# Optimization experiments

Measured on AMD Instinct MI355X. Metric: run time of the kernel, lower is better.

## Reference

```python
import jax, jax.numpy as jnp
import numpy as np

H = 4          # attention heads
C = 64         # per-head channels (hidden_size)
NEG_SLOPE = 0.2  # PyG GATConv default negative_slope


def _gat_layer(x, W, a_src, a_dst, b, src, dst):
    """PyG-style GATConv (concat=True) on one graph. x: [N, F]."""
    N = x.shape[0]
    h = (x @ W).reshape(N, H, C)                      # [N, H, C]
    s_src = jnp.sum(h * a_src, axis=-1)               # [N, H]
    s_dst = jnp.sum(h * a_dst, axis=-1)               # [N, H]
    e = jax.nn.leaky_relu(s_src[src] + s_dst[dst], NEG_SLOPE)   # [E, H]
    # softmax over incoming edges of each destination node
    m = jax.ops.segment_max(e, dst, num_segments=N)   # [N, H]
    m = jnp.where(jnp.isfinite(m), m, 0.0)
    ex = jnp.exp(e - m[dst])
    denom = jax.ops.segment_sum(ex, dst, num_segments=N)
    alpha = ex / denom[dst]                           # [E, H]
    out = jax.ops.segment_sum(h[src] * alpha[:, :, None], dst, num_segments=N)
    return out.reshape(N, H * C) + b                  # [N, H*C]


def setup_inputs() -> dict:
    key = jax.random.key(0)
    ks = jax.random.split(key, 12)
    B, N, F = 2, 20000, 128
    E = 320000
    HC = H * C  # 256
    x = jax.random.normal(ks[0], (B, N, F), dtype=jnp.float32)
    edge_index = jax.random.randint(ks[1], (2, E), 0, N, dtype=jnp.int64)
    def glorot(k, shape):
        fan = shape[0] + shape[-1]
        return jax.random.normal(k, shape, dtype=jnp.float32) * np.sqrt(2.0 / fan)
    return {
        "x": x,
        "edge_index": edge_index,
        "W1": glorot(ks[2], (F, HC)),
        "a_src1": glorot(ks[3], (H, C)),
        "a_dst1": glorot(ks[4], (H, C)),
        "b1": jnp.zeros((HC,), jnp.float32),
        "W2": glorot(ks[5], (HC, HC)),
        "a_src2": glorot(ks[6], (H, C)),
        "a_dst2": glorot(ks[7], (H, C)),
        "b2": jnp.zeros((HC,), jnp.float32),
        "Wf": glorot(ks[8], (HC, C)),
        "bf": jnp.zeros((C,), jnp.float32),
    }


def reference(x, edge_index, W1, a_src1, a_dst1, b1, W2, a_src2, a_dst2, b2, Wf, bf):
    B, N, _ = x.shape
    sl = jnp.arange(N, dtype=edge_index.dtype)        # self loops (PyG default)
    src = jnp.concatenate([edge_index[0], sl])
    dst = jnp.concatenate([edge_index[1], sl])
    h = jax.vmap(lambda xi: _gat_layer(xi, W1, a_src1, a_dst1, b1, src, dst))(x)
    h = jax.nn.elu(h)
    h = jax.vmap(lambda xi: _gat_layer(xi, W2, a_src2, a_dst2, b2, src, dst))(h)
    return h @ Wf + bf                                 # [B, N, hidden]
```

## Files before the change

kernel.cpp:

```cpp
#include <hip/hip_runtime.h>
#include <math.h>

#define NN 20000
#define NE 320000
#define ETOT (NE + NN)
#define NH 4
#define CH 64
#define HC 256
#define FIN 128
#define NEG_SLOPE 0.2f
#define CAP 64
#define EST 80
#define SCB 79

typedef unsigned short ushort_t;
typedef unsigned int uint_t;
typedef _Float16 half8 __attribute__((ext_vector_type(8)));
typedef float f32x4 __attribute__((ext_vector_type(4)));

__device__ __forceinline__ ushort_t f2h_bits(float f) {
    union { _Float16 h; ushort_t u; } c; c.h = (_Float16)f;
    return c.u;
}

__device__ __forceinline__ void fma_mix_pair(float& alo, float& ahi, uint_t word, float w) {
    asm("v_fma_mix_f32 %0, %1, %2, %0 op_sel:[0,0,0] op_sel_hi:[1,0,0]"
        : "+v"(alo) : "v"(word), "v"(w));
    asm("v_fma_mix_f32 %0, %1, %2, %0 op_sel:[1,0,0] op_sel_hi:[1,0,0]"
        : "+v"(ahi) : "v"(word), "v"(w));
}


#define HB ((ETOT + 255) / 256)
#define SN1 (FIN * HC)
#define SN2 (SN1 + HC * HC)
#define SN3 (SN2 + HC * CH)
#define SN4 (SN3 + (2 * NN * FIN) / 4)
#define SB ((SN4 + 255) / 256)

__global__ void k_hist_setup(const int* __restrict__ ei, int* __restrict__ counts,
                             const float* __restrict__ x, const float* __restrict__ W1,
                             const float* __restrict__ W2, const float* __restrict__ Wf,
                             ushort_t* __restrict__ Xh, ushort_t* __restrict__ Wt1,
                             ushort_t* __restrict__ Wt2, ushort_t* __restrict__ Wtf) {
    int blk = blockIdx.x;
    if (blk < HB) {
        int e = blk * 256 + threadIdx.x;
        if (e >= ETOT) return;
        int d = (e < NE) ? ei[NE + e] : (e - NE);
        atomicAdd(&counts[d], 1);
    } else {
        int i = (blk - HB) * 256 + threadIdx.x;
        if (i < SN1) {
            int n = i / FIN, k = i - n * FIN;
            Wt1[i] = f2h_bits(W1[(size_t)k * HC + n]);
        } else if (i < SN2) {
            int j = i - SN1;
            int n = j / HC, k = j - n * HC;
            Wt2[j] = f2h_bits(W2[(size_t)k * HC + n]);
        } else if (i < SN3) {
            int j = i - SN2;
            int n = j / HC, k = j - n * HC;
            Wtf[j] = f2h_bits(Wf[(size_t)k * CH + n]);
        } else if (i < SN4) {
            int j = (i - SN3) * 4;
            float4 v = *reinterpret_cast<const float4*>(&x[j]);
            ushort4 u;
            u.x = f2h_bits(v.x); u.y = f2h_bits(v.y); u.z = f2h_bits(v.z); u.w = f2h_bits(v.w);
            *reinterpret_cast<ushort4*>(&Xh[j]) = u;
        }
    }
}


__global__ void k_scan_part(const int* __restrict__ counts, int* __restrict__ bsum) {
    __shared__ int red[256];
    int t = threadIdx.x;
    int i = blockIdx.x * 256 + t;
    red[t] = (i < NN) ? counts[i] : 0;
    __syncthreads();
#pragma unroll
    for (int off = 128; off > 0; off >>= 1) {
        if (t < off) red[t] += red[t + off];
        __syncthreads();
    }
    if (t == 0) bsum[blockIdx.x] = red[0];
}

__global__ void k_scan_top(const int* __restrict__ bsum, int* __restrict__ bpre) {
    __shared__ int s[128];
    int t = threadIdx.x;
    int own = (t < SCB) ? bsum[t] : 0;
    s[t] = own;
    __syncthreads();
#pragma unroll
    for (int off = 1; off < 128; off <<= 1) {
        int v = (t >= off) ? s[t - off] : 0;
        __syncthreads();
        s[t] += v;
        __syncthreads();
    }
    if (t < SCB) bpre[t] = s[t] - own;
}

__global__ void k_scan_apply(const int* __restrict__ counts, const int* __restrict__ bpre,
                             int* __restrict__ rowptr, int* __restrict__ cursor) {
    __shared__ int s[256];
    int t = threadIdx.x;
    int i = blockIdx.x * 256 + t;
    int c = (i < NN) ? counts[i] : 0;
    s[t] = c;
    __syncthreads();
#pragma unroll
    for (int off = 1; off < 256; off <<= 1) {
        int v = (t >= off) ? s[t - off] : 0;
        __syncthreads();
        s[t] += v;
        __syncthreads();
    }
    int ex = s[t] - c + bpre[blockIdx.x];
    if (i < NN) { rowptr[i] = ex; cursor[i] = ex; }
    if (i == NN - 1) rowptr[NN] = ex + c;
}

__global__ void k_scatter(const int* __restrict__ ei, int* __restrict__ cursor,
                          int* __restrict__ col) {
    int e = blockIdx.x * blockDim.x + threadIdx.x;
    if (e >= ETOT) return;
    int s, d;
    if (e < NE) { s = ei[e]; d = ei[NE + e]; }
    else        { s = e - NE; d = s; }
    int pos = atomicAdd(&cursor[d], 1);
    col[pos] = s;
}


__global__ __launch_bounds__(256) void k_gemm128(const ushort_t* __restrict__ A,
                                                 const ushort_t* __restrict__ Bt,
                                                 ushort_t* __restrict__ Ch,
                                                 const float* __restrict__ a_src,
                                                 const float* __restrict__ a_dst,
                                                 float* __restrict__ ssrc,
                                                 float* __restrict__ sdst,
                                                 int M, int K, int NC) {
    __shared__ ushort_t As[128 * 40];
    __shared__ ushort_t Bs[128 * 40];
    int tid = threadIdx.x;
    int wave = tid >> 6, lane = tid & 63;
    int wr = wave >> 1, wc = wave & 1;
    int row0 = blockIdx.x * 128, col0 = blockIdx.y * 128;

    f32x4 acc[4][4];
#pragma unroll
    for (int i = 0; i < 4; ++i)
#pragma unroll
        for (int j = 0; j < 4; ++j) acc[i][j] = (f32x4){0.f, 0.f, 0.f, 0.f};

    int srow = tid >> 2;
    int sk8 = (tid & 3) * 8;
    int l15 = lane & 15, lk = (lane >> 4) * 8;

    int ra0 = min(row0 + srow, M - 1);
    int ra1 = min(row0 + 64 + srow, M - 1);

    for (int k0 = 0; k0 < K; k0 += 32) {
        uint4 a0 = *reinterpret_cast<const uint4*>(&A[(size_t)ra0 * K + k0 + sk8]);
        uint4 a1 = *reinterpret_cast<const uint4*>(&A[(size_t)ra1 * K + k0 + sk8]);
        uint4 b0 = *reinterpret_cast<const uint4*>(&Bt[(size_t)(col0 + srow) * K + k0 + sk8]);
        uint4 b1 = *reinterpret_cast<const uint4*>(&Bt[(size_t)(col0 + 64 + srow) * K + k0 + sk8]);
        __syncthreads();
        *reinterpret_cast<uint4*>(&As[srow * 40 + sk8]) = a0;
        *reinterpret_cast<uint4*>(&As[(64 + srow) * 40 + sk8]) = a1;
        *reinterpret_cast<uint4*>(&Bs[srow * 40 + sk8]) = b0;
        *reinterpret_cast<uint4*>(&Bs[(64 + srow) * 40 + sk8]) = b1;
        __syncthreads();

        half8 af[4], bf_[4];
#pragma unroll
        for (int m = 0; m < 4; ++m)
            af[m] = *reinterpret_cast<const half8*>(&As[(wr * 64 + m * 16 + l15) * 40 + lk]);
#pragma unroll
        for (int nf = 0; nf < 4; ++nf)
            bf_[nf] = *reinterpret_cast<const half8*>(&Bs[(wc * 64 + nf * 16 + l15) * 40 + lk]);
#pragma unroll
        for (int m = 0; m < 4; ++m)
#pragma unroll
            for (int nf = 0; nf < 4; ++nf)
                acc[m][nf] = __builtin_amdgcn_mfma_f32_16x16x32_f16(af[m], bf_[nf], acc[m][nf], 0, 0, 0);
    }

#pragma unroll
    for (int m = 0; m < 4; ++m)
#pragma unroll
        for (int nf = 0; nf < 4; ++nf) {
            int colc = col0 + wc * 64 + nf * 16 + l15;
#pragma unroll
            for (int j = 0; j < 4; ++j) {
                int row = row0 + wr * 64 + m * 16 + (lane >> 4) * 4 + j;
                if (row < M) Ch[(size_t)row * NC + colc] = f2h_bits(acc[m][nf][j]);
            }
        }

    if (ssrc) {
        int head = (col0 >> 6) + wc;
        float as4[4], ad4[4];
#pragma unroll
        for (int nf = 0; nf < 4; ++nf) {
            as4[nf] = a_src[head * 64 + nf * 16 + l15];
            ad4[nf] = a_dst[head * 64 + nf * 16 + l15];
        }
#pragma unroll
        for (int m = 0; m < 4; ++m)
#pragma unroll
            for (int j = 0; j < 4; ++j) {
                float ps = acc[m][0][j] * as4[0] + acc[m][1][j] * as4[1]
                         + acc[m][2][j] * as4[2] + acc[m][3][j] * as4[3];
                float pd = acc[m][0][j] * ad4[0] + acc[m][1][j] * ad4[1]
                         + acc[m][2][j] * ad4[2] + acc[m][3][j] * ad4[3];
#pragma unroll
                for (int off = 1; off < 16; off <<= 1) {
                    ps += __shfl_xor(ps, off);
                    pd += __shfl_xor(pd, off);
                }
                int row = row0 + wr * 64 + m * 16 + (lane >> 4) * 4 + j;
                if (l15 == 0 && row < M) {
                    ssrc[(size_t)row * NH + head] = ps;
                    sdst[(size_t)row * NH + head] = pd;
                }
            }
    }
}


__global__ __launch_bounds__(256) void k_gemm_mfma(const ushort_t* __restrict__ A,
                                                   const ushort_t* __restrict__ Bt,
                                                   float* __restrict__ Cf,
                                                   const float* __restrict__ bias,
                                                   int M, int K, int NC) {
    __shared__ ushort_t As[64][40];
    __shared__ ushort_t Bs[64][40];
    int tid = threadIdx.x;
    int wave = tid >> 6, lane = tid & 63;
    int wr = wave >> 1, wc = wave & 1;
    int row0 = blockIdx.x * 64, col0 = blockIdx.y * 64;

    f32x4 acc[2][2];
#pragma unroll
    for (int i = 0; i < 2; ++i)
#pragma unroll
        for (int j = 0; j < 2; ++j) acc[i][j] = (f32x4){0.f, 0.f, 0.f, 0.f};

    int sr = tid >> 2;
    int sk = (tid & 3) * 8;
    int l15 = lane & 15, lk = (lane >> 4) * 8;

    for (int k0 = 0; k0 < K; k0 += 32) {
        uint4 av = make_uint4(0, 0, 0, 0);
        int rowg = row0 + sr;
        if (rowg < M) av = *reinterpret_cast<const uint4*>(&A[(size_t)rowg * K + k0 + sk]);
        uint4 bv = *reinterpret_cast<const uint4*>(&Bt[(size_t)(col0 + sr) * K + k0 + sk]);
        __syncthreads();
        *reinterpret_cast<uint4*>(&As[sr][sk]) = av;
        *reinterpret_cast<uint4*>(&Bs[sr][sk]) = bv;
        __syncthreads();

        half8 a0 = *reinterpret_cast<const half8*>(&As[wr * 32 + l15][lk]);
        half8 a1 = *reinterpret_cast<const half8*>(&As[wr * 32 + 16 + l15][lk]);
        half8 b0 = *reinterpret_cast<const half8*>(&Bs[wc * 32 + l15][lk]);
        half8 b1 = *reinterpret_cast<const half8*>(&Bs[wc * 32 + 16 + l15][lk]);
        acc[0][0] = __builtin_amdgcn_mfma_f32_16x16x32_f16(a0, b0, acc[0][0], 0, 0, 0);
        acc[0][1] = __builtin_amdgcn_mfma_f32_16x16x32_f16(a0, b1, acc[0][1], 0, 0, 0);
        acc[1][0] = __builtin_amdgcn_mfma_f32_16x16x32_f16(a1, b0, acc[1][0], 0, 0, 0);
        acc[1][1] = __builtin_amdgcn_mfma_f32_16x16x32_f16(a1, b1, acc[1][1], 0, 0, 0);
    }

#pragma unroll
    for (int fr = 0; fr < 2; ++fr)
#pragma unroll
        for (int fc = 0; fc < 2; ++fc) {
            int colc = col0 + wc * 32 + fc * 16 + l15;
#pragma unroll
            for (int j = 0; j < 4; ++j) {
                int row = row0 + wr * 32 + fr * 16 + (lane >> 4) * 4 + j;
                if (row < M) Cf[(size_t)row * NC + colc] = acc[fr][fc][j] + bias[colc];
            }
        }
}


__global__ __launch_bounds__(256) void k_agg(const ushort_t* __restrict__ hb,
                                             const float* __restrict__ ssrc,
                                             const float* __restrict__ sdst,
                                             const int* __restrict__ rowptr,
                                             const int* __restrict__ col,
                                             const float* __restrict__ bias,
                                             ushort_t* __restrict__ outh,
                                             int do_elu) {
    __shared__ int cols_lds[4][CAP];
    __shared__ float e_lds[4][4 * EST];
    __shared__ float den_lds[4][4];
    int wave = threadIdx.x >> 6, lane = threadIdx.x & 63;
    int gw = blockIdx.x * 4 + wave;
    int b = (gw >= NN) ? 1 : 0;
    int n = gw - b * NN;
    int* colw = cols_lds[wave];
    float* ew = e_lds[wave];
    int start = rowptr[n];
    int deg = rowptr[n + 1] - start;
    int es = lane >> 5;
    int cg = lane & 31;
    int hd = cg >> 3;
    int ea = lane >> 2;
    int ha = lane & 3;

    const ushort_t* hbase = hb + (size_t)b * NN * HC;
    const float* ssrcb = ssrc + (size_t)b * NN * NH;

    float sdh = sdst[((size_t)b * NN + n) * NH + ha];

    float pdp = 0.f;
    float acc[8];
#pragma unroll
    for (int j = 0; j < 8; ++j) acc[j] = 0.f;

    const int cg8 = cg * 8;

    for (int c0 = 0; c0 < deg; c0 += CAP) {
        int cnt = min(CAP, deg - c0);
        int cnt8 = (cnt + 7) & ~7;

        for (int i0 = 0; i0 < cnt8; i0 += 16) {
            int i = i0 + ea;
            if (i < cnt) {
                int s = col[start + c0 + i];
                if (ha == 0) colw[i] = s * HC;
                float e = ssrcb[(size_t)s * NH + ha] + sdh;
                e = fmaxf(e, NEG_SLOPE * e);
                float w = __expf(e);
                ew[ha * EST + i] = w;
                pdp += w;
            } else {
                if (ha == 0) colw[i] = 0;
                ew[ha * EST + i] = 0.f;
            }
        }

        for (int i = 0; i < cnt8; i += 8) {
            int i0 = i + es, i1 = i + 2 + es, i2 = i + 4 + es, i3 = i + 6 + es;
            int o0 = colw[i0], o1 = colw[i1], o2 = colw[i2], o3 = colw[i3];
            float w0 = ew[hd * EST + i0], w1 = ew[hd * EST + i1];
            float w2 = ew[hd * EST + i2], w3 = ew[hd * EST + i3];
            uint4 u0 = *reinterpret_cast<const uint4*>(hbase + o0 + cg8);
            uint4 u1 = *reinterpret_cast<const uint4*>(hbase + o1 + cg8);
            uint4 u2 = *reinterpret_cast<const uint4*>(hbase + o2 + cg8);
            uint4 u3 = *reinterpret_cast<const uint4*>(hbase + o3 + cg8);
            fma_mix_pair(acc[0], acc[1], u0.x, w0);
            fma_mix_pair(acc[2], acc[3], u0.y, w0);
            fma_mix_pair(acc[4], acc[5], u0.z, w0);
            fma_mix_pair(acc[6], acc[7], u0.w, w0);
            fma_mix_pair(acc[0], acc[1], u1.x, w1);
            fma_mix_pair(acc[2], acc[3], u1.y, w1);
            fma_mix_pair(acc[4], acc[5], u1.z, w1);
            fma_mix_pair(acc[6], acc[7], u1.w, w1);
            fma_mix_pair(acc[0], acc[1], u2.x, w2);
            fma_mix_pair(acc[2], acc[3], u2.y, w2);
            fma_mix_pair(acc[4], acc[5], u2.z, w2);
            fma_mix_pair(acc[6], acc[7], u2.w, w2);
            fma_mix_pair(acc[0], acc[1], u3.x, w3);
            fma_mix_pair(acc[2], acc[3], u3.y, w3);
            fma_mix_pair(acc[4], acc[5], u3.z, w3);
            fma_mix_pair(acc[6], acc[7], u3.w, w3);
        }
    }

#pragma unroll
    for (int off = 4; off < 64; off <<= 1) pdp += __shfl_xor(pdp, off);
    if (lane < 4) den_lds[wave][ha] = pdp;

#pragma unroll
    for (int j = 0; j < 8; ++j) acc[j] += __shfl_xor(acc[j], 32);

    if (es == 0) {
        float inv = 1.0f / den_lds[wave][hd];
        float4 b0 = *reinterpret_cast<const float4*>(&bias[cg8]);
        float4 b1 = *reinterpret_cast<const float4*>(&bias[cg8 + 4]);
        float bv[8] = {b0.x, b0.y, b0.z, b0.w, b1.x, b1.y, b1.z, b1.w};
        ushort_t o[8];
#pragma unroll
        for (int j = 0; j < 8; ++j) {
            float r = acc[j] * inv + bv[j];
            if (do_elu && r < 0.f) r = expm1f(r);
            o[j] = f2h_bits(r);
        }
        *reinterpret_cast<uint4*>(&outh[((size_t)b * NN + n) * HC + cg8]) =
            *reinterpret_cast<uint4*>(&o[0]);
    }
}


extern "C" void kernel_launch(void* const* d_in, const int* in_sizes, int n_in,
                              void* d_out, int out_size, void* d_ws, size_t ws_size,
                              hipStream_t stream) {
    const float* x      = (const float*)d_in[0];
    const int*   ei     = (const int*)d_in[1];
    const float* W1     = (const float*)d_in[2];
    const float* a_src1 = (const float*)d_in[3];
    const float* a_dst1 = (const float*)d_in[4];
    const float* b1     = (const float*)d_in[5];
    const float* W2     = (const float*)d_in[6];
    const float* a_src2 = (const float*)d_in[7];
    const float* a_dst2 = (const float*)d_in[8];
    const float* b2     = (const float*)d_in[9];
    const float* Wf     = (const float*)d_in[10];
    const float* bf     = (const float*)d_in[11];
    float* out = (float*)d_out;

    const int M2 = 2 * NN;
    float* ws = (float*)d_ws;
    float* Ssrc = ws;
    float* Sdst = Ssrc + (size_t)M2 * NH;
    ushort_t* Hb16 = (ushort_t*)(Sdst + (size_t)M2 * NH);
    ushort_t* Ob16 = Hb16 + (size_t)M2 * HC;
    ushort_t* Xb16 = Ob16 + (size_t)M2 * HC;
    ushort_t* Wt1  = Xb16 + (size_t)M2 * FIN;
    ushort_t* Wt2  = Wt1 + (size_t)HC * FIN;
    ushort_t* Wtf  = Wt2 + (size_t)HC * HC;
    int* counts = (int*)(Wtf + (size_t)CH * HC);
    int* rowptr = counts + NN;
    int* cursor = rowptr + (NN + 1);
    int* colidx = cursor + NN;
    int* bsum   = colidx + ETOT;
    int* bpre   = bsum + SCB;

    hipMemsetAsync(counts, 0, (size_t)NN * sizeof(int), stream);
    k_hist_setup<<<HB + SB, 256, 0, stream>>>(ei, counts, x, W1, W2, Wf,
                                              Xb16, Wt1, Wt2, Wtf);
    k_scan_part<<<SCB, 256, 0, stream>>>(counts, bsum);
    k_scan_top<<<1, 128, 0, stream>>>(bsum, bpre);
    k_scan_apply<<<SCB, 256, 0, stream>>>(counts, bpre, rowptr, cursor);
    k_scatter<<<(ETOT + 255) / 256, 256, 0, stream>>>(ei, cursor, colidx);

    const int gM128 = (M2 + 127) / 128;
    const int gAgg = M2 / 4;
    k_gemm128<<<dim3(gM128, HC / 128), 256, 0, stream>>>(Xb16, Wt1, Hb16, a_src1, a_dst1,
                                                         Ssrc, Sdst, M2, FIN, HC);
    k_agg<<<gAgg, 256, 0, stream>>>(Hb16, Ssrc, Sdst, rowptr, colidx, b1, Ob16, 1);
    k_gemm128<<<dim3(gM128, HC / 128), 256, 0, stream>>>(Ob16, Wt2, Hb16, a_src2, a_dst2,
                                                         Ssrc, Sdst, M2, HC, HC);
    k_agg<<<gAgg, 256, 0, stream>>>(Hb16, Ssrc, Sdst, rowptr, colidx, b2, Ob16, 0);
    k_gemm_mfma<<<dim3((M2 + 63) / 64, CH / 64), 256, 0, stream>>>(Ob16, Wtf, out, bf, M2, HC, CH);
}
```

Baseline: 184.8 us.

## Fuse x fp16 conversion into layer-1 GEMM and co-launch with edge scatter

Removes the separate pass that converts x to fp16; the first GEMM now reads fp32 x directly and packs it to half in registers. The edge scatter and the layer-1 GEMM are merged into one launch, with block index ranges split between the two jobs, which saves a launch and lets them run concurrently. The aggregation inner loop is also cut from 8-edge to 4-edge steps with padding to a multiple of 4, reducing wasted padded work on low-degree nodes at the cost of less memory-level parallelism per iteration.

```diff
diff --git a/kernel.cpp b/kernel.cpp
--- a/kernel.cpp
+++ b/kernel.cpp
@@ -12,6 +12,7 @@
 #define CAP 64
 #define EST 80
 #define SCB 79
+#define GM128 313
 
 typedef unsigned short ushort_t;
 typedef unsigned int uint_t;
@@ -21,6 +22,9 @@
 __device__ __forceinline__ ushort_t f2h_bits(float f) {
     union { _Float16 h; ushort_t u; } c; c.h = (_Float16)f;
     return c.u;
+}
+__device__ __forceinline__ uint_t pack2h(float a, float b) {
+    return (uint_t)f2h_bits(a) | ((uint_t)f2h_bits(b) << 16);
 }
 
 __device__ __forceinline__ void fma_mix_pair(float& alo, float& ahi, uint_t word, float w) {
@@ -35,13 +39,11 @@
 #define SN1 (FIN * HC)
 #define SN2 (SN1 + HC * HC)
 #define SN3 (SN2 + HC * CH)
-#define SN4 (SN3 + (2 * NN * FIN) / 4)
-#define SB ((SN4 + 255) / 256)
+#define SB ((SN3 + 255) / 256)
 
 __global__ void k_hist_setup(const int* __restrict__ ei, int* __restrict__ counts,
-                             const float* __restrict__ x, const float* __restrict__ W1,
-                             const float* __restrict__ W2, const float* __restrict__ Wf,
-                             ushort_t* __restrict__ Xh, ushort_t* __restrict__ Wt1,
+                             const float* __restrict__ W1, const float* __restrict__ W2,
+                             const float* __restrict__ Wf, ushort_t* __restrict__ Wt1,
                              ushort_t* __restrict__ Wt2, ushort_t* __restrict__ Wtf) {
     int blk = blockIdx.x;
     if (blk < HB) {
@@ -62,12 +64,6 @@
             int j = i - SN2;
             int n = j / HC, k = j - n * HC;
             Wtf[j] = f2h_bits(Wf[(size_t)k * CH + n]);
-        } else if (i < SN4) {
-            int j = (i - SN3) * 4;
-            float4 v = *reinterpret_cast<const float4*>(&x[j]);
-            ushort4 u;
-            u.x = f2h_bits(v.x); u.y = f2h_bits(v.y); u.z = f2h_bits(v.z); u.w = f2h_bits(v.w);
-            *reinterpret_cast<ushort4*>(&Xh[j]) = u;
         }
     }
 }
@@ -123,32 +119,22 @@
     if (i == NN - 1) rowptr[NN] = ex + c;
 }
 
-__global__ void k_scatter(const int* __restrict__ ei, int* __restrict__ cursor,
-                          int* __restrict__ col) {
-    int e = blockIdx.x * blockDim.x + threadIdx.x;
-    if (e >= ETOT) return;
-    int s, d;
-    if (e < NE) { s = ei[e]; d = ei[NE + e]; }
-    else        { s = e - NE; d = s; }
-    int pos = atomicAdd(&cursor[d], 1);
-    col[pos] = s;
-}
-
-
-__global__ __launch_bounds__(256) void k_gemm128(const ushort_t* __restrict__ A,
-                                                 const ushort_t* __restrict__ Bt,
-                                                 ushort_t* __restrict__ Ch,
-                                                 const float* __restrict__ a_src,
-                                                 const float* __restrict__ a_dst,
-                                                 float* __restrict__ ssrc,
-                                                 float* __restrict__ sdst,
-                                                 int M, int K, int NC) {
-    __shared__ ushort_t As[128 * 40];
-    __shared__ ushort_t Bs[128 * 40];
+
+__device__ __forceinline__ void gemm128_body(const ushort_t* __restrict__ A,
+                                             const float* __restrict__ Af,
+                                             const ushort_t* __restrict__ Bt,
+                                             ushort_t* __restrict__ Ch,
+                                             const float* __restrict__ a_src,
+                                             const float* __restrict__ a_dst,
+                                             float* __restrict__ ssrc,
+                                             float* __restrict__ sdst,
+                                             int M, int K, int NC, int row0, int col0,
+                                             ushort_t* S) {
+    ushort_t* As = S;
+    ushort_t* Bs = S + 128 * 40;
     int tid = threadIdx.x;
     int wave = tid >> 6, lane = tid & 63;
     int wr = wave >> 1, wc = wave & 1;
-    int row0 = blockIdx.x * 128, col0 = blockIdx.y * 128;
 
     f32x4 acc[4][4];
 #pragma unroll
@@ -164,8 +150,22 @@
     int ra1 = min(row0 + 64 + srow, M - 1);
 
     for (int k0 = 0; k0 < K; k0 += 32) {
-        uint4 a0 = *reinterpret_cast<const uint4*>(&A[(size_t)ra0 * K + k0 + sk8]);
-        uint4 a1 = *reinterpret_cast<const uint4*>(&A[(size_t)ra1 * K + k0 + sk8]);
+        uint4 a0, a1;
+        if (Af) {
+            const float* p0 = &Af[(size_t)ra0 * K + k0 + sk8];
+            float4 f0 = *reinterpret_cast<const float4*>(p0);
+            float4 f1 = *reinterpret_cast<const float4*>(p0 + 4);
+            a0 = make_uint4(pack2h(f0.x, f0.y), pack2h(f0.z, f0.w),
+                            pack2h(f1.x, f1.y), pack2h(f1.z, f1.w));
+            const float* p1 = &Af[(size_t)ra1 * K + k0 + sk8];
+            float4 g0 = *reinterpret_cast<const float4*>(p1);
+            float4 g1 = *reinterpret_cast<const float4*>(p1 + 4);
+            a1 = make_uint4(pack2h(g0.x, g0.y), pack2h(g0.z, g0.w),
+                            pack2h(g1.x, g1.y), pack2h(g1.z, g1.w));
+        } else {
+            a0 = *reinterpret_cast<const uint4*>(&A[(size_t)ra0 * K + k0 + sk8]);
+            a1 = *reinterpret_cast<const uint4*>(&A[(size_t)ra1 * K + k0 + sk8]);
+        }
         uint4 b0 = *reinterpret_cast<const uint4*>(&Bt[(size_t)(col0 + srow) * K + k0 + sk8]);
         uint4 b1 = *reinterpret_cast<const uint4*>(&Bt[(size_t)(col0 + 64 + srow) * K + k0 + sk8]);
         __syncthreads();
@@ -228,6 +228,48 @@
                     sdst[(size_t)row * NH + head] = pd;
                 }
             }
+    }
+}
+
+__global__ __launch_bounds__(256) void k_gemm128(const ushort_t* __restrict__ A,
+                                                 const ushort_t* __restrict__ Bt,
+                                                 ushort_t* __restrict__ Ch,
+                                                 const float* __restrict__ a_src,
+                                                 const float* __restrict__ a_dst,
+                                                 float* __restrict__ ssrc,
+                                                 float* __restrict__ sdst,
+                                                 int M, int K, int NC) {
+    __shared__ ushort_t S[2 * 128 * 40];
+    gemm128_body(A, nullptr, Bt, Ch, a_src, a_dst, ssrc, sdst, M, K, NC,
+                 blockIdx.x * 128, blockIdx.y * 128, S);
+}
+
+__global__ __launch_bounds__(256) void k_scatter_gemm1(const int* __restrict__ ei,
+                                                       int* __restrict__ cursor,
+                                                       int* __restrict__ col,
+                                                       const float* __restrict__ xf,
+                                                       const ushort_t* __restrict__ Bt,
+                                                       ushort_t* __restrict__ Ch,
+                                                       const float* __restrict__ a_src,
+                                                       const float* __restrict__ a_dst,
+                                                       float* __restrict__ ssrc,
+                                                       float* __restrict__ sdst,
+                                                       int M) {
+    __shared__ ushort_t S[2 * 128 * 40];
+    if (blockIdx.x < HB) {
+        int e = blockIdx.x * 256 + threadIdx.x;
+        if (e >= ETOT) return;
+        int s, d;
+        if (e < NE) { s = ei[e]; d = ei[NE + e]; }
+        else        { s = e - NE; d = s; }
+        int pos = atomicAdd(&cursor[d], 1);
+        col[pos] = s;
+    } else {
+        int g = blockIdx.x - HB;
+        int row0 = (g % GM128) * 128;
+        int col0 = (g / GM128) * 128;
+        gemm128_body(nullptr, xf, Bt, Ch, a_src, a_dst, ssrc, sdst, M, FIN, HC,
+                     row0, col0, S);
     }
 }
 
@@ -327,9 +369,9 @@
 
     for (int c0 = 0; c0 < deg; c0 += CAP) {
         int cnt = min(CAP, deg - c0);
-        int cnt8 = (cnt + 7) & ~7;
-
-        for (int i0 = 0; i0 < cnt8; i0 += 16) {
+        int cnt4 = (cnt + 3) & ~3;
+
+        for (int i0 = 0; i0 < cnt4; i0 += 16) {
             int i = i0 + ea;
             if (i < cnt) {
                 int s = col[start + c0 + i];
@@ -345,15 +387,12 @@
             }
         }
 
-        for (int i = 0; i < cnt8; i += 8) {
-            int i0 = i + es, i1 = i + 2 + es, i2 = i + 4 + es, i3 = i + 6 + es;
-            int o0 = colw[i0], o1 = colw[i1], o2 = colw[i2], o3 = colw[i3];
+        for (int i = 0; i < cnt4; i += 4) {
+            int i0 = i + es, i1 = i + 2 + es;
+            int o0 = colw[i0], o1 = colw[i1];
             float w0 = ew[hd * EST + i0], w1 = ew[hd * EST + i1];
-            float w2 = ew[hd * EST + i2], w3 = ew[hd * EST + i3];
             uint4 u0 = *reinterpret_cast<const uint4*>(hbase + o0 + cg8);
             uint4 u1 = *reinterpret_cast<const uint4*>(hbase + o1 + cg8);
-            uint4 u2 = *reinterpret_cast<const uint4*>(hbase + o2 + cg8);
-            uint4 u3 = *reinterpret_cast<const uint4*>(hbase + o3 + cg8);
             fma_mix_pair(acc[0], acc[1], u0.x, w0);
             fma_mix_pair(acc[2], acc[3], u0.y, w0);
             fma_mix_pair(acc[4], acc[5], u0.z, w0);
@@ -362,14 +401,6 @@
             fma_mix_pair(acc[2], acc[3], u1.y, w1);
             fma_mix_pair(acc[4], acc[5], u1.z, w1);
             fma_mix_pair(acc[6], acc[7], u1.w, w1);
-            fma_mix_pair(acc[0], acc[1], u2.x, w2);
-            fma_mix_pair(acc[2], acc[3], u2.y, w2);
-            fma_mix_pair(acc[4], acc[5], u2.z, w2);
-            fma_mix_pair(acc[6], acc[7], u2.w, w2);
-            fma_mix_pair(acc[0], acc[1], u3.x, w3);
-            fma_mix_pair(acc[2], acc[3], u3.y, w3);
-            fma_mix_pair(acc[4], acc[5], u3.z, w3);
-            fma_mix_pair(acc[6], acc[7], u3.w, w3);
         }
     }
 
@@ -433,19 +464,16 @@
     int* bpre   = bsum + SCB;
 
     hipMemsetAsync(counts, 0, (size_t)NN * sizeof(int), stream);
-    k_hist_setup<<<HB + SB, 256, 0, stream>>>(ei, counts, x, W1, W2, Wf,
-                                              Xb16, Wt1, Wt2, Wtf);
+    k_hist_setup<<<HB + SB, 256, 0, stream>>>(ei, counts, W1, W2, Wf, Wt1, Wt2, Wtf);
     k_scan_part<<<SCB, 256, 0, stream>>>(counts, bsum);
     k_scan_top<<<1, 128, 0, stream>>>(bsum, bpre);
     k_scan_apply<<<SCB, 256, 0, stream>>>(counts, bpre, rowptr, cursor);
-    k_scatter<<<(ETOT + 255) / 256, 256, 0, stream>>>(ei, cursor, colidx);
-
-    const int gM128 = (M2 + 127) / 128;
+
     const int gAgg = M2 / 4;
-    k_gemm128<<<dim3(gM128, HC / 128), 256, 0, stream>>>(Xb16, Wt1, Hb16, a_src1, a_dst1,
-                                                         Ssrc, Sdst, M2, FIN, HC);
+    k_scatter_gemm1<<<HB + GM128 * (HC / 128), 256, 0, stream>>>(
+        ei, cursor, colidx, x, Wt1, Hb16, a_src1, a_dst1, Ssrc, Sdst, M2);
     k_agg<<<gAgg, 256, 0, stream>>>(Hb16, Ssrc, Sdst, rowptr, colidx, b1, Ob16, 1);
-    k_gemm128<<<dim3(gM128, HC / 128), 256, 0, stream>>>(Ob16, Wt2, Hb16, a_src2, a_dst2,
+    k_gemm128<<<dim3(GM128, HC / 128), 256, 0, stream>>>(Ob16, Wt2, Hb16, a_src2, a_dst2,
                                                          Ssrc, Sdst, M2, HC, HC);
     k_agg<<<gAgg, 256, 0, stream>>>(Hb16, Ssrc, Sdst, rowptr, colidx, b2, Ob16, 0);
     k_gemm_mfma<<<dim3((M2 + 63) / 64, CH / 64), 256, 0, stream>>>(Ob16, Wtf, out, bf, M2, HC, CH);
```

After: 188.5 us. +2.0%, slower.
